# Kernel tuning notes

Hardware: AMD Instinct MI355X
Metric: run time of the kernel (lower is better)

The kernel has to match this reference:

```python
import jax, jax.numpy as jnp
import numpy as np

BATCH, SEQ, IN, HID = 64, 2048, 256, 256


def setup_inputs() -> dict:
    key = jax.random.key(0)
    ks = jax.random.split(key, 9)
    x = jax.random.normal(ks[0], (BATCH, SEQ, IN), dtype=jnp.float32)
    scale_i = (6.0 / (IN + HID)) ** 0.5   # xavier_uniform bound for (IN,HID)
    scale_h = (6.0 / (HID + HID)) ** 0.5  # xavier_uniform bound for (HID,HID)
    def wi(k):
        return jax.random.uniform(k, (IN, HID), dtype=jnp.float32, minval=-scale_i, maxval=scale_i)
    def wh(k):
        return jax.random.uniform(k, (HID, HID), dtype=jnp.float32, minval=-scale_h, maxval=scale_h)
    z = jnp.zeros((HID,), dtype=jnp.float32)
    return {
        "x": x,
        "W_ii": wi(ks[1]), "W_hi": wh(ks[2]), "b_ii": z, "b_hi": z,
        "W_if": wi(ks[3]), "W_hf": wh(ks[4]), "b_if": z, "b_hf": z,
        "W_ig": wi(ks[5]), "W_hg": wh(ks[6]), "b_ig": z, "b_hg": z,
        "W_io": wi(ks[7]), "W_ho": wh(ks[8]), "b_io": z, "b_ho": z,
    }


def reference(x, W_ii, W_hi, b_ii, b_hi, W_if, W_hf, b_if, b_hf,
              W_ig, W_hg, b_ig, b_hg, W_io, W_ho, b_io, b_ho):
    bs, seq, _ = x.shape
    hid = W_hi.shape[0]
    # Precompute all input projections in one pass (same math as per-step matmuls).
    # xi/xf/xg/xo: [bs, seq, hid]
    xi = x @ W_ii + b_ii + b_hi
    xf = x @ W_if + b_if + b_hf
    xg = x @ W_ig + b_ig + b_hg
    xo = x @ W_io + b_io + b_ho
    # Stack as [seq, bs, hid] for scan over time.
    xs = jnp.stack([xi, xf, xg, xo], axis=0).transpose(2, 0, 1, 3)  # [seq,4,bs,hid]

    def step(carry, x_t):
        h, c = carry
        pi, pf, pg, po = x_t[0], x_t[1], x_t[2], x_t[3]
        i_t = jax.nn.sigmoid(pi + h @ W_hi)
        f_t = jax.nn.sigmoid(pf + h @ W_hf)
        g_t = jnp.tanh(pg + h @ W_hg)
        o_t = jax.nn.sigmoid(po + h @ W_ho)
        c_new = f_t * c + i_t * g_t
        h_new = o_t * jnp.tanh(c_new)
        return (h_new, c_new), None

    h0 = jnp.zeros((bs, hid), dtype=x.dtype)
    c0 = jnp.zeros((bs, hid), dtype=x.dtype)
    (h_t, c_t), _ = jax.lax.scan(step, (h0, c0), xs)
    return (h_t, c_t)
```

## Files before the change

### kernel.cpp

```cpp
#include <hip/hip_runtime.h>
#include <hip/hip_bf16.h>
#include <stdint.h>

#define BATCH 64
#define SEQ   2048
#define KDIM  256
#define HIDD  256

#define LOG2E 1.44269504f

typedef __attribute__((ext_vector_type(8))) short short8;
typedef __attribute__((ext_vector_type(4))) float f32x4;
typedef __attribute__((ext_vector_type(2))) unsigned int uint2v;
typedef __attribute__((ext_vector_type(4))) float f32x4v;
typedef __attribute__((ext_vector_type(4))) int int4v;

#define WSCALE 1172.0f
#define DQF    (1.0f / (127.0f * 1172.0f))
#define DQFS   (-(LOG2E) * DQF)
#define DQFG2  (-2.0f * (LOG2E) * DQF)
#define CNEG   (-2.0f * LOG2E)

__device__ __forceinline__ float fexp2(float x) {
#if __has_builtin(__builtin_amdgcn_exp2f)
    return __builtin_amdgcn_exp2f(x);
#else
    return exp2f(x);
#endif
}
__device__ __forceinline__ float frcp(float x) {
#if __has_builtin(__builtin_amdgcn_rcpf)
    return __builtin_amdgcn_rcpf(x);
#else
    return 1.0f / x;
#endif
}

__device__ __forceinline__ int dot4(int a, int b, int c) {
#if __has_builtin(__builtin_amdgcn_sdot4)
    return __builtin_amdgcn_sdot4(a, b, c, false);
#else
    int s = c;
    s += ((a << 24) >> 24) * ((b << 24) >> 24);
    s += ((a << 16) >> 24) * ((b << 16) >> 24);
    s += ((a << 8)  >> 24) * ((b << 8)  >> 24);
    s += (a >> 24) * (b >> 24);
    return s;
#endif
}

#if __has_builtin(__builtin_amdgcn_update_dpp)
#define XOR1_I(x) __builtin_amdgcn_update_dpp(0, (x), 0xB1, 0xF, 0xF, true)
#define XOR2_I(x) __builtin_amdgcn_update_dpp(0, (x), 0x4E, 0xF, 0xF, true)
#else
#define XOR1_I(x) __shfl_xor((x), 1, 64)
#define XOR2_I(x) __shfl_xor((x), 2, 64)
#endif
__device__ __forceinline__ float xor1_f(float x) {
    return __int_as_float(XOR1_I(__float_as_int(x)));
}
__device__ __forceinline__ float xor2_f(float x) {
    return __int_as_float(XOR2_I(__float_as_int(x)));
}

__device__ __forceinline__ unsigned short f32_to_bf16_rne(float f) {
    union { float f; uint32_t u; } v; v.f = f;
    uint32_t u = v.u;
    uint32_t r = (u + 0x7FFFu + ((u >> 16) & 1u)) >> 16;
    return (unsigned short)r;
}
__device__ __forceinline__ float bf16_to_f32(unsigned short h) {
    union { float f; uint32_t u; } v; v.u = ((uint32_t)h) << 16;
    return v.f;
}

struct PrepArgs {
    const float* Wi[4];
    const float* Wh[4];
    const float* bi[4];
    const float* bh[4];
    unsigned short* WT;
    float* biascat;
    int* Wh8;
};

__global__ __launch_bounds__(256) void prep_kernel(PrepArgs a) {
    int blk = blockIdx.x, tid = threadIdx.x;
    if (blk < 512) {
        int TT = blk >> 3;
        int kt = blk & 7;
        int w  = TT >> 4, nn = TT & 15;
        int L  = tid >> 2;
        int ep = (tid & 3) * 2;
        int k0 = kt * 32 + (L >> 4) * 8 + ep;
        int j  = nn * 16 + (L & 15);
        const float* Wg = a.Wi[w];
        unsigned short b0 = f32_to_bf16_rne(Wg[(size_t)(k0 + 0) * 256 + j]);
        unsigned short b1 = f32_to_bf16_rne(Wg[(size_t)(k0 + 1) * 256 + j]);
        uint32_t pk = (uint32_t)b0 | ((uint32_t)b1 << 16);
        ((uint32_t*)a.WT)[(((blk * 64 + L) * 8) + ep) >> 1] = pk;
    } else if (blk < 516) {
        int n = (blk - 512) * 256 + tid;
        int g = n >> 8, j = n & 255;
        a.biascat[n] = a.bi[g][j] + a.bh[g][j];
    } else if (blk < 772) {
        int gq = blk - 516;
        int g = gq >> 6, kq = gq & 63;
        int j = tid;
        const float* Wg = a.Wh[g];
        uint32_t dw = 0;
#pragma unroll
        for (int i = 0; i < 4; ++i) {
            float wv = Wg[(size_t)(kq * 4 + i) * 256 + j];
            float s = fminf(fmaxf(wv * WSCALE, -127.f), 127.f);
            int q8 = __float2int_rn(s);
            dw |= ((uint32_t)(uint8_t)(int8_t)q8) << (i * 8);
        }
        a.Wh8[gq * 256 + j] = (int)dw;
    }
}

__global__ __launch_bounds__(256, 2) void proj_kernel(
        const float* __restrict__ x,
        const unsigned short* __restrict__ WT,
        const float* __restrict__ biascat,
        uint32_t* __restrict__ Psw) {
    const int t    = blockIdx.x >> 1;
    const int half = blockIdx.x & 1;
    const int w    = threadIdx.x >> 6;
    const int L    = threadIdx.x & 63;

    __shared__ unsigned short xt[32][272];

    {
        const int r = threadIdx.x >> 3;
        const int qq = threadIdx.x & 7;
        const float* xr = x + ((size_t)(half * 32 + r) * SEQ + t) * KDIM;
#pragma unroll
        for (int it = 0; it < 8; ++it) {
            int c = qq * 4 + it * 32;
            f32x4v v = __builtin_nontemporal_load((const f32x4v*)(xr + c));
            xt[r][c + 0] = f32_to_bf16_rne(v.x);
            xt[r][c + 1] = f32_to_bf16_rne(v.y);
            xt[r][c + 2] = f32_to_bf16_rne(v.z);
            xt[r][c + 3] = f32_to_bf16_rne(v.w);
        }
    }
    __syncthreads();

    f32x4 acc[2][16];
#pragma unroll
    for (int m = 0; m < 2; ++m)
#pragma unroll
        for (int nn = 0; nn < 16; ++nn) acc[m][nn] = (f32x4){0.f, 0.f, 0.f, 0.f};

#pragma unroll
    for (int kt = 0; kt < 8; ++kt) {
        const int kc = kt * 32 + ((L >> 4) * 8);
        short8 a0 = *(const short8*)&xt[(L & 15)][kc];
        short8 a1 = *(const short8*)&xt[16 + (L & 15)][kc];
#pragma unroll
        for (int nn = 0; nn < 16; ++nn) {
            const short8 bf = *(const short8*)(WT +
                ((size_t)(((w * 16 + nn) * 8 + kt) * 64 + L)) * 8);
            acc[0][nn] = __builtin_amdgcn_mfma_f32_16x16x32_bf16(a0, bf, acc[0][nn], 0, 0, 0);
            acc[1][nn] = __builtin_amdgcn_mfma_f32_16x16x32_bf16(a1, bf, acc[1][nn], 0, 0, 0);
        }
    }

    const float sg = (w == 2) ? (-2.0f * LOG2E) : (-LOG2E);

#pragma unroll
    for (int mt2 = 0; mt2 < 2; ++mt2) {
        const int bg = half * 2 + mt2;
#pragma unroll
        for (int nn = 0; nn < 16; ++nn) {
            float bv = biascat[w * 256 + nn * 16 + (L & 15)];
            unsigned short r0 = f32_to_bf16_rne((acc[mt2][nn][0] + bv) * sg);
            unsigned short r1 = f32_to_bf16_rne((acc[mt2][nn][1] + bv) * sg);
            unsigned short r2 = f32_to_bf16_rne((acc[mt2][nn][2] + bv) * sg);
            unsigned short r3 = f32_to_bf16_rne((acc[mt2][nn][3] + bv) * sg);
            uint2v pk;
            pk.x = (uint32_t)r0 | ((uint32_t)r1 << 16);
            pk.y = (uint32_t)r2 | ((uint32_t)r3 << 16);
            size_t off_dw = (((size_t)t * 4 + bg) * 8 + (w * 2 + (nn & 1))) * 1024
                          + (size_t)((nn >> 1) * 64 + L) * 2;
            *(uint2v*)(Psw + off_dw) = pk;
        }
    }
}

__global__ __launch_bounds__(1024, 4) void recur_kernel(
        const int* __restrict__ Wp2,
        const uint32_t* __restrict__ Psw,
        float* __restrict__ out) {
    const int b = blockIdx.x;
    const int T = threadIdx.x;
    const int j = T >> 2;
    const int q = T & 3;

    __shared__ __align__(16) int hq[2][64];

    int Wreg[4][16];
#pragma unroll
    for (int m = 0; m < 4; ++m)
#pragma unroll
        for (int kq = 0; kq < 16; ++kq)
            Wreg[m][kq] = Wp2[((q ^ m) * 64 + q * 16 + kq) * 256 + j];

    if (T < 128) ((int*)hq)[T] = 0;

    const int baseq = (b >> 4) * 8192 + q * 2048 + ((j >> 4) & 1) * 1024
                    + (j >> 5) * 128 + ((b >> 2) & 3) * 32 + (j & 15) * 2
                    + ((b & 3) >> 1);
    const int psh = (b & 1) * 16;

    uint32_t prefA = Psw[baseq];
    uint32_t prefB = Psw[32768 + baseq];

    const float dqf  = (q == 2) ? DQFG2 : DQFS;
    const float vsc  = (q == 2) ? 2.f : 1.f;
    const float voff = (q == 2) ? -1.f : 0.f;

    float c_st = 0.f, h_last = 0.f;

    __syncthreads();

#define LSTM_STEP(TT, PREF, HRD, HWR)                                          \
    {                                                                          \
        uint32_t myp = PREF;                                                   \
        if ((TT) + 2 < SEQ)                                                    \
            PREF = Psw[(size_t)((TT) + 2) * 32768 + baseq];                    \
        int p0 = 0, p1 = 0, p2 = 0, p3 = 0;                                    \
        const int4v* h4 = (const int4v*)((HRD) + q * 16);                      \
        _Pragma("unroll")                                                      \
        for (int k4 = 0; k4 < 4; ++k4) {                                       \
            int4v hb = h4[k4];                                                 \
            _Pragma("unroll")                                                  \
            for (int r = 0; r < 4; ++r) {                                      \
                int hh = hb[r];                                                \
                p0 = dot4(hh, Wreg[0][k4 * 4 + r], p0);                        \
                p1 = dot4(hh, Wreg[1][k4 * 4 + r], p1);                        \
                p2 = dot4(hh, Wreg[2][k4 * 4 + r], p2);                        \
                p3 = dot4(hh, Wreg[3][k4 * 4 + r], p3);                        \
            }                                                                  \
        }                                                                      \
        int r0 = p0 + XOR1_I(p1);                                              \
        int r2 = p2 + XOR1_I(p3);                                              \
        int f0 = r0 + XOR2_I(r2);          \
        float pre = (float)f0 * dqf + bf16_to_f32((unsigned short)(myp >> psh)); \
        float sg1 = frcp(1.f + fexp2(pre));                                    \
        float vv  = sg1 * vsc + voff;           \
        float mm  = vv * xor2_f(vv);                           \
        float mx  = xor1_f(mm);                              \
        float cn  = vv * c_st + mx;                      \
        c_st = cn;                                                             \
        float th  = 2.f * frcp(1.f + fexp2(cn * CNEG)) - 1.f;       \
        float hout = vv * xor2_f(th);                    \
        h_last = hout;                                                         \
        if (q == 3)                                                            \
            ((char*)(HWR))[j] = (char)__float2int_rn(hout * 127.f);            \
        __syncthreads();                                                       \
    }

    int* h0b = hq[0];
    int* h1b = hq[1];

    for (int t = 0; t < SEQ; t += 2) {
        LSTM_STEP(t,     prefA, h0b, h1b);
        LSTM_STEP(t + 1, prefB, h1b, h0b);
    }
#undef LSTM_STEP

    if (q == 3) out[(size_t)b * 256 + j]         = h_last;
    if (q == 1) out[16384 + (size_t)b * 256 + j] = c_st;
}

extern "C" void kernel_launch(void* const* d_in, const int* in_sizes, int n_in,
                              void* d_out, int out_size, void* d_ws, size_t ws_size,
                              hipStream_t stream) {
    (void)in_sizes; (void)n_in; (void)out_size; (void)ws_size;
    const float* x = (const float*)d_in[0];

    char* ws = (char*)d_ws;
    const size_t PSW_BYTES = (size_t)SEQ * 4 * 8192 * 4;
    uint32_t*       Psw     = (uint32_t*)ws;
    unsigned short* WT      = (unsigned short*)(ws + PSW_BYTES);
    int*            Wh8     = (int*)(ws + PSW_BYTES + 524288);
    float*          biascat = (float*)(ws + PSW_BYTES + 524288 + 262144);

    PrepArgs pa;
    pa.Wi[0] = (const float*)d_in[1];  pa.Wh[0] = (const float*)d_in[2];
    pa.bi[0] = (const float*)d_in[3];  pa.bh[0] = (const float*)d_in[4];
    pa.Wi[1] = (const float*)d_in[5];  pa.Wh[1] = (const float*)d_in[6];
    pa.bi[1] = (const float*)d_in[7];  pa.bh[1] = (const float*)d_in[8];
    pa.Wi[2] = (const float*)d_in[9];  pa.Wh[2] = (const float*)d_in[10];
    pa.bi[2] = (const float*)d_in[11]; pa.bh[2] = (const float*)d_in[12];
    pa.Wi[3] = (const float*)d_in[13]; pa.Wh[3] = (const float*)d_in[14];
    pa.bi[3] = (const float*)d_in[15]; pa.bh[3] = (const float*)d_in[16];
    pa.WT = WT; pa.biascat = biascat; pa.Wh8 = Wh8;
    prep_kernel<<<772, 256, 0, stream>>>(pa);

    proj_kernel<<<4096, 256, 0, stream>>>(x, WT, biascat, Psw);

    recur_kernel<<<64, 1024, 0, stream>>>((const int*)Wh8, Psw, (float*)d_out);
}
```

Baseline: 2.062 ms.

## Fuse input projection into recurrent kernel with per-16-step LDS bursts

Removes the separate projection kernel and its large global Psw buffer. The recurrent kernel now computes each batch row's input projections for 16 timesteps at a time with MFMA into a double-buffered LDS tile, interleaved with the serial LSTM steps. The per-step __syncthreads is also replaced by an explicit waitcnt plus s_barrier. This cuts global traffic and a launch, but adds MFMA work and x loads inside the serial critical path of only 64 blocks, which may stall the recurrence.

```diff
diff --git a/kernel.cpp b/kernel.cpp
--- a/kernel.cpp
+++ b/kernel.cpp
@@ -120,86 +120,22 @@
     }
 }
 
-__global__ __launch_bounds__(256, 2) void proj_kernel(
-        const float* __restrict__ x,
-        const unsigned short* __restrict__ WT,
-        const float* __restrict__ biascat,
-        uint32_t* __restrict__ Psw) {
-    const int t    = blockIdx.x >> 1;
-    const int half = blockIdx.x & 1;
-    const int w    = threadIdx.x >> 6;
-    const int L    = threadIdx.x & 63;
-
-    __shared__ unsigned short xt[32][272];
-
-    {
-        const int r = threadIdx.x >> 3;
-        const int qq = threadIdx.x & 7;
-        const float* xr = x + ((size_t)(half * 32 + r) * SEQ + t) * KDIM;
-#pragma unroll
-        for (int it = 0; it < 8; ++it) {
-            int c = qq * 4 + it * 32;
-            f32x4v v = __builtin_nontemporal_load((const f32x4v*)(xr + c));
-            xt[r][c + 0] = f32_to_bf16_rne(v.x);
-            xt[r][c + 1] = f32_to_bf16_rne(v.y);
-            xt[r][c + 2] = f32_to_bf16_rne(v.z);
-            xt[r][c + 3] = f32_to_bf16_rne(v.w);
-        }
-    }
-    __syncthreads();
-
-    f32x4 acc[2][16];
-#pragma unroll
-    for (int m = 0; m < 2; ++m)
-#pragma unroll
-        for (int nn = 0; nn < 16; ++nn) acc[m][nn] = (f32x4){0.f, 0.f, 0.f, 0.f};
-
-#pragma unroll
-    for (int kt = 0; kt < 8; ++kt) {
-        const int kc = kt * 32 + ((L >> 4) * 8);
-        short8 a0 = *(const short8*)&xt[(L & 15)][kc];
-        short8 a1 = *(const short8*)&xt[16 + (L & 15)][kc];
-#pragma unroll
-        for (int nn = 0; nn < 16; ++nn) {
-            const short8 bf = *(const short8*)(WT +
-                ((size_t)(((w * 16 + nn) * 8 + kt) * 64 + L)) * 8);
-            acc[0][nn] = __builtin_amdgcn_mfma_f32_16x16x32_bf16(a0, bf, acc[0][nn], 0, 0, 0);
-            acc[1][nn] = __builtin_amdgcn_mfma_f32_16x16x32_bf16(a1, bf, acc[1][nn], 0, 0, 0);
-        }
-    }
-
-    const float sg = (w == 2) ? (-2.0f * LOG2E) : (-LOG2E);
-
-#pragma unroll
-    for (int mt2 = 0; mt2 < 2; ++mt2) {
-        const int bg = half * 2 + mt2;
-#pragma unroll
-        for (int nn = 0; nn < 16; ++nn) {
-            float bv = biascat[w * 256 + nn * 16 + (L & 15)];
-            unsigned short r0 = f32_to_bf16_rne((acc[mt2][nn][0] + bv) * sg);
-            unsigned short r1 = f32_to_bf16_rne((acc[mt2][nn][1] + bv) * sg);
-            unsigned short r2 = f32_to_bf16_rne((acc[mt2][nn][2] + bv) * sg);
-            unsigned short r3 = f32_to_bf16_rne((acc[mt2][nn][3] + bv) * sg);
-            uint2v pk;
-            pk.x = (uint32_t)r0 | ((uint32_t)r1 << 16);
-            pk.y = (uint32_t)r2 | ((uint32_t)r3 << 16);
-            size_t off_dw = (((size_t)t * 4 + bg) * 8 + (w * 2 + (nn & 1))) * 1024
-                          + (size_t)((nn >> 1) * 64 + L) * 2;
-            *(uint2v*)(Psw + off_dw) = pk;
-        }
-    }
-}
-
 __global__ __launch_bounds__(1024, 4) void recur_kernel(
         const int* __restrict__ Wp2,
-        const uint32_t* __restrict__ Psw,
+        const unsigned short* __restrict__ WTf,
+        const float* __restrict__ biascat,
+        const float* __restrict__ x,
         float* __restrict__ out) {
-    const int b = blockIdx.x;
-    const int T = threadIdx.x;
-    const int j = T >> 2;
-    const int q = T & 3;
+    const int b  = blockIdx.x;
+    const int T  = threadIdx.x;
+    const int j  = T >> 2;
+    const int q  = T & 3;
+    const int wv = T >> 6;
+    const int L  = T & 63;
 
     __shared__ __align__(16) int hq[2][64];
+    __shared__ __align__(16) unsigned short Pl[2][16 * 1044];
+    __shared__ __align__(16) unsigned short xs[16][264];
 
     int Wreg[4][16];
 #pragma unroll
@@ -210,27 +146,60 @@
 
     if (T < 128) ((int*)hq)[T] = 0;
 
-    const int baseq = (b >> 4) * 8192 + q * 2048 + ((j >> 4) & 1) * 1024
-                    + (j >> 5) * 128 + ((b >> 2) & 3) * 32 + (j & 15) * 2
-                    + ((b & 3) >> 1);
-    const int psh = (b & 1) * 16;
-
-    uint32_t prefA = Psw[baseq];
-    uint32_t prefB = Psw[32768 + baseq];
-
+    float bv[4], sgl[4];
+#pragma unroll
+    for (int nn = 0; nn < 4; ++nn) {
+        int n = (wv * 4 + nn) * 16 + (L & 15);
+        bv[nn]  = biascat[n];
+        sgl[nn] = ((n >> 8) == 2) ? (-2.0f * LOG2E) : (-LOG2E);
+    }
+
+    const int pcol = j * 4 + q;
     const float dqf  = (q == 2) ? DQFG2 : DQFS;
     const float vsc  = (q == 2) ? 2.f : 1.f;
     const float voff = (q == 2) ? -1.f : 0.f;
-
     float c_st = 0.f, h_last = 0.f;
 
-    __syncthreads();
-
-#define LSTM_STEP(TT, PREF, HRD, HWR)                                          \
+#define STAGE_X(TW1) { \
+        int row = T >> 6; int c0 = (T & 63) * 4; \
+        f32x4v v = *(const f32x4v*)(x + ((size_t)b * SEQ + (size_t)(TW1) * 16 + row) * KDIM + c0); \
+        uint2v u; \
+        u.x = (uint32_t)f32_to_bf16_rne(v.x) | ((uint32_t)f32_to_bf16_rne(v.y) << 16); \
+        u.y = (uint32_t)f32_to_bf16_rne(v.z) | ((uint32_t)f32_to_bf16_rne(v.w) << 16); \
+        *(uint2v*)&xs[row][c0] = u; }
+
+#define BURST(TW1) { \
+        unsigned short* Pb = Pl[(TW1) & 1]; \
+        _Pragma("unroll") \
+        for (int pair = 0; pair < 2; ++pair) { \
+            f32x4 ac0 = (f32x4){0.f, 0.f, 0.f, 0.f}; \
+            f32x4 ac1 = (f32x4){0.f, 0.f, 0.f, 0.f}; \
+            const int TT0 = wv * 4 + pair * 2; \
+            _Pragma("unroll") \
+            for (int kt = 0; kt < 8; ++kt) { \
+                short8 av = *(const short8*)&xs[L & 15][kt * 32 + (L >> 4) * 8]; \
+                short8 bf0 = *(const short8*)(WTf + ((size_t)((TT0 * 8 + kt) * 64 + L)) * 8); \
+                short8 bf1 = *(const short8*)(WTf + ((size_t)(((TT0 + 1) * 8 + kt) * 64 + L)) * 8); \
+                ac0 = __builtin_amdgcn_mfma_f32_16x16x32_bf16(av, bf0, ac0, 0, 0, 0); \
+                ac1 = __builtin_amdgcn_mfma_f32_16x16x32_bf16(av, bf1, ac1, 0, 0, 0); \
+            } \
+            _Pragma("unroll") \
+            for (int nn2 = 0; nn2 < 2; ++nn2) { \
+                f32x4 ac = nn2 ? ac1 : ac0; \
+                int nn = pair * 2 + nn2; \
+                int n = (wv * 4 + nn) * 16 + (L & 15); \
+                int bhw = (n & 255) * 4 + (n >> 8); \
+                _Pragma("unroll") \
+                for (int reg = 0; reg < 4; ++reg) { \
+                    int r = (L >> 4) * 4 + reg; \
+                    Pb[r * 1044 + bhw] = \
+                        f32_to_bf16_rne((ac[reg] + bv[nn]) * sgl[nn]); \
+                } \
+            } \
+        } }
+
+#define LSTM_STEP(PBASE, HRD, HWR)                                             \
     {                                                                          \
-        uint32_t myp = PREF;                                                   \
-        if ((TT) + 2 < SEQ)                                                    \
-            PREF = Psw[(size_t)((TT) + 2) * 32768 + baseq];                    \
         int p0 = 0, p1 = 0, p2 = 0, p3 = 0;                                    \
         const int4v* h4 = (const int4v*)((HRD) + q * 16);                      \
         _Pragma("unroll")                                                      \
@@ -248,7 +217,8 @@
         int r0 = p0 + XOR1_I(p1);                                              \
         int r2 = p2 + XOR1_I(p3);                                              \
         int f0 = r0 + XOR2_I(r2);          \
-        float pre = (float)f0 * dqf + bf16_to_f32((unsigned short)(myp >> psh)); \
+        float pm = bf16_to_f32((PBASE)[pcol]);                                 \
+        float pre = (float)f0 * dqf + pm;                                      \
         float sg1 = frcp(1.f + fexp2(pre));                                    \
         float vv  = sg1 * vsc + voff;           \
         float mm  = vv * xor2_f(vv);                           \
@@ -260,17 +230,37 @@
         h_last = hout;                                                         \
         if (q == 3)                                                            \
             ((char*)(HWR))[j] = (char)__float2int_rn(hout * 127.f);            \
-        __syncthreads();                                                       \
-    }
+        asm volatile("" ::: "memory");                                         \
+        __builtin_amdgcn_s_waitcnt(0xC07F);                    \
+        __builtin_amdgcn_s_barrier();                                          \
+        asm volatile("" ::: "memory");                                         \
+    }
+
+    __syncthreads();
+
+    STAGE_X(0)
+    __syncthreads();
+    BURST(0)
+    __syncthreads();
 
     int* h0b = hq[0];
     int* h1b = hq[1];
 
-    for (int t = 0; t < SEQ; t += 2) {
-        LSTM_STEP(t,     prefA, h0b, h1b);
-        LSTM_STEP(t + 1, prefB, h1b, h0b);
+    for (int tw = 0; tw < 128; ++tw) {
+        if (tw + 1 < 128) {
+            STAGE_X(tw + 1)
+            __syncthreads();
+            BURST(tw + 1)
+        }
+        unsigned short* Pcur = Pl[tw & 1];
+        for (int s = 0; s < 16; s += 2) {
+            LSTM_STEP(Pcur + (size_t)s * 1044,       h0b, h1b)
+            LSTM_STEP(Pcur + (size_t)(s + 1) * 1044, h1b, h0b)
+        }
     }
 #undef LSTM_STEP
+#undef BURST
+#undef STAGE_X
 
     if (q == 3) out[(size_t)b * 256 + j]         = h_last;
     if (q == 1) out[16384 + (size_t)b * 256 + j] = c_st;
@@ -283,11 +273,9 @@
     const float* x = (const float*)d_in[0];
 
     char* ws = (char*)d_ws;
-    const size_t PSW_BYTES = (size_t)SEQ * 4 * 8192 * 4;
-    uint32_t*       Psw     = (uint32_t*)ws;
-    unsigned short* WT      = (unsigned short*)(ws + PSW_BYTES);
-    int*            Wh8     = (int*)(ws + PSW_BYTES + 524288);
-    float*          biascat = (float*)(ws + PSW_BYTES + 524288 + 262144);
+    unsigned short* WT      = (unsigned short*)ws;
+    int*            Wh8     = (int*)(ws + 524288);
+    float*          biascat = (float*)(ws + 524288 + 262144);
 
     PrepArgs pa;
     pa.Wi[0] = (const float*)d_in[1];  pa.Wh[0] = (const float*)d_in[2];
@@ -301,7 +289,6 @@
     pa.WT = WT; pa.biascat = biascat; pa.Wh8 = Wh8;
     prep_kernel<<<772, 256, 0, stream>>>(pa);
 
-    proj_kernel<<<4096, 256, 0, stream>>>(x, WT, biascat, Psw);
-
-    recur_kernel<<<64, 1024, 0, stream>>>((const int*)Wh8, Psw, (float*)d_out);
-}
+    recur_kernel<<<64, 1024, 0, stream>>>((const int*)Wh8, WT, biascat, x,
+                                          (float*)d_out);
+}
```

After: 2.929 ms. 1.42x slower.
